# Optimization experiments

Hardware: AMD Instinct MI355X
Metric: run time of the kernel (lower is better)

Reference implementation:

```python
import jax, jax.numpy as jnp
import numpy as np

B, S, D, V, K, H, L, U = 256, 50, 32, 10000, 16, 64, 2, 32
NORM = 0.01


def setup_inputs() -> dict:
    key = jax.random.key(0)
    ks = iter(jax.random.split(key, 64))
    r = lambda *sh: jax.random.normal(next(ks), sh, dtype=jnp.float32) * 0.05
    inp = {
        'x1': r(B, U), 'z1': r(B, S, D), 'x2': r(B, U), 'z2': r(B, S, D),
        'embd': r(V, D),
        'dec_w1': r(D, H), 'dec_b1': r(H), 'dec_w2': r(H, D), 'dec_b2': r(D),
        'i_wih': r(3 * D, D), 'i_whh': r(3 * D, D), 'i_bih': r(3 * D), 'i_bhh': r(3 * D),
        'c_wih': r(3 * D, D), 'c_whh': r(3 * D, D), 'c_bih': r(3 * D), 'c_bhh': r(3 * D),
        'im_w1': r(D, D), 'im_b1': r(D), 'im_w2': r(D, D), 'im_b2': r(D),
        'cm_w1': r(D, D), 'cm_b1': r(D), 'cm_w2': r(D, D), 'cm_b2': r(D),
        'hw1': r(L, D, K * K), 'hb1': r(L, K * K), 'hw2': r(L, D, K * K), 'hb2': r(L, K * K),
        'lin_w': r(L, U, K), 'lin_b': r(L, K), 'lout_w': r(L, K, U), 'lout_b': r(L, U),
        'sample_num': B, 'trigger_seq_length': 30,
    }
    return inp


def _gru(x, wih, whh, bih, bhh):
    # PyTorch GRU, batch_first, h0 = 0; gate order (r, z, n)
    gi = jnp.einsum('bsd,ed->bse', x, wih) + bih  # [B,S,3D]

    def step(h, gi_t):
        gh = h @ whh.T + bhh
        gir, giz, gin = jnp.split(gi_t, 3, axis=-1)
        ghr, ghz, ghn = jnp.split(gh, 3, axis=-1)
        rr = jax.nn.sigmoid(gir + ghr)
        zz = jax.nn.sigmoid(giz + ghz)
        nn = jnp.tanh(gin + rr * ghn)
        h = (1.0 - zz) * nn + zz * h
        return h, h

    h0 = jnp.zeros((x.shape[0], whh.shape[1]), x.dtype)
    _, hs = jax.lax.scan(step, h0, jnp.swapaxes(gi, 0, 1))
    return jnp.swapaxes(hs, 0, 1)  # [B,S,D]


def _forward(x1, z1, x2, z2, embd, dec_w1, dec_b1, dec_w2, dec_b2,
             i_wih, i_whh, i_bih, i_bhh, c_wih, c_whh, c_bih, c_bhh,
             im_w1, im_b1, im_w2, im_b2, cm_w1, cm_b1, cm_w2, cm_b2,
             hw1, hb1, hw2, hb2, lin_w, lin_b, lout_w, lout_b,
             sample_num, trigger_seq_length):
    # --- VQVAE.find_nearest: cdist + argmin + gather (index path has no grad) ---
    q = jax.lax.stop_gradient(z1)
    t = jax.lax.stop_gradient(embd)
    # ||q - t||^2 expanded; argmin over sqrt == argmin over squared dist
    d2 = ((q * q).sum(-1)[:, :, None]
          - 2.0 * jnp.einsum('bsd,vd->bsv', q, t)
          + (t * t).sum(-1)[None, None, :])  # [B,S,V]
    idx = jnp.argmin(d2, axis=2)  # [B,S]
    z_emb = embd[idx]  # [B,S,D], gradient flows into embd via gather

    # --- VQVAE.decode ---
    h = jax.nn.leaky_relu(z_emb @ dec_w1 + dec_b1, negative_slope=0.1)
    z_recon = h @ dec_w2 + dec_b2  # [B,S,D]

    total_loss = jnp.mean((z2 - jax.lax.stop_gradient(z_emb)) ** 2)

    # --- item branch: GRU -> pick trigger step -> MLP (tanh, linear) ---
    hs = _gru(z_recon, i_wih, i_whh, i_bih, i_bhh)
    u1 = hs[:, trigger_seq_length, :]
    z1f = jnp.tanh(u1 @ im_w1 + im_b1) @ im_w2 + im_b2  # [B,D]

    # --- category branch ---
    hs = _gru(z2, c_wih, c_whh, c_bih, c_bhh)
    u2 = hs[:, trigger_seq_length, :]
    z2f = jnp.tanh(u2 @ cm_w1 + cm_b1) @ cm_w2 + cm_b2  # [B,D]

    # --- hypernetwork layers (activations in self.modules are never applied) ---
    out = x1
    for i in range(L):
        iw = (z1f @ hw1[i] + hb1[i]).reshape(sample_num, K, K)
        cw = (z2f @ hw2[i] + hb2[i]).reshape(sample_num, K, K)
        w = jnp.clip(iw, -NORM, NORM) + cw  # [B,K,K]
        out = out @ lin_w[i] + lin_b[i]  # [B,K]
        out = jnp.einsum('bk,bkj->bj', out, w)  # bmm
        out = out @ lout_w[i] + lout_b[i]  # [B,U]
    return out, total_loss


def reference(x1, z1, x2, z2, embd, dec_w1, dec_b1, dec_w2, dec_b2,
              i_wih, i_whh, i_bih, i_bhh, c_wih, c_whh, c_bih, c_bhh,
              im_w1, im_b1, im_w2, im_b2, cm_w1, cm_b1, cm_w2, cm_b2,
              hw1, hb1, hw2, hb2, lin_w, lin_b, lout_w, lout_b,
              sample_num, trigger_seq_length):
    return _forward(x1, z1, x2, z2, embd, dec_w1, dec_b1, dec_w2, dec_b2,
                    i_wih, i_whh, i_bih, i_bhh, c_wih, c_whh, c_bih, c_bhh,
                    im_w1, im_b1, im_w2, im_b2, cm_w1, cm_b1, cm_w2, cm_b2,
                    hw1, hb1, hw2, hb2, lin_w, lin_b, lout_w, lout_b,
                    sample_num, trigger_seq_length)
```

## Files before the change

### kernel.cpp

```cpp
#include <hip/hip_runtime.h>
#include <math.h>

#define B 256
#define S 50
#define D 32
#define V 10000
#define VPAD 10240
#define KK 16
#define HH 64
#define LL 2
#define UU 32
#define TT 30
#define NROWS (B*S)
#define NORMC 0.01f
#define CH 256
#define NSLICE 10
#define SLICE_V 1024
#define VQ_RB 128

typedef __attribute__((ext_vector_type(8))) short bf16x8;
typedef __attribute__((ext_vector_type(4))) float f32x4;

__device__ __forceinline__ float sigmoidf_(float x) { return 1.0f / (1.0f + expf(-x)); }

__device__ __forceinline__ unsigned short f2bf(float x) {
    union { float f; unsigned int u; } a; a.f = x;
    unsigned int u = a.u;
    return (unsigned short)((u + 0x7FFFu + ((u >> 16) & 1u)) >> 16);
}
__device__ __forceinline__ float bf2f(unsigned short h) {
    union { unsigned int u; float f; } a; a.u = ((unsigned int)h) << 16; return a.f;
}

__device__ __forceinline__ void gld16(void* lds, const void* g) {
    __builtin_amdgcn_global_load_lds(
        (const __attribute__((address_space(1))) unsigned int*)g,
        (__attribute__((address_space(3))) unsigned int*)lds, 16, 0, 0);
}
__device__ __forceinline__ void gld4(void* lds, const void* g) {
    __builtin_amdgcn_global_load_lds(
        (const __attribute__((address_space(1))) unsigned int*)g,
        (__attribute__((address_space(3))) unsigned int*)lds, 4, 0, 0);
}

__global__ __launch_bounds__(256) void k_prep(const float* __restrict__ embd,
                                              const float* __restrict__ z1,
                                              unsigned short* __restrict__ Eh, unsigned short* __restrict__ El,
                                              unsigned short* __restrict__ Qh, unsigned short* __restrict__ Ql,
                                              float* __restrict__ tn, float* __restrict__ loss_sum,
                                              unsigned int* __restrict__ cnt) {
    int gid = blockIdx.x * 256 + threadIdx.x;
    if (gid == 0) loss_sum[0] = 0.f;
    if (gid == 1) cnt[0] = 0u;
    if (gid >= VPAD * 4 + 4 * NROWS) return;
    int isRow = (gid >= VPAD * 4);
    if (!isRow) {
        int item = gid >> 2, qd = gid & 3;
        unsigned short* dh = Eh + (size_t)item * D + qd * 8;
        unsigned short* dl = El + (size_t)item * D + qd * 8;
        if (item >= V) {
            unsigned short z[8] = {0, 0, 0, 0, 0, 0, 0, 0};
            *(uint4*)dh = *(const uint4*)z;
            *(uint4*)dl = *(const uint4*)z;
            if (qd == 0) tn[item] = INFINITY;
            return;
        }
        const float* src = embd + (size_t)item * D + qd * 8;
        float4 x0 = *(const float4*)(src);
        float4 x1 = *(const float4*)(src + 4);
        float xs[8] = {x0.x, x0.y, x0.z, x0.w, x1.x, x1.y, x1.z, x1.w};
        unsigned short hv[8], lv[8];
        float ss = 0.f;
#pragma unroll
        for (int i = 0; i < 8; i++) {
            float x = xs[i];
            ss = fmaf(x, x, ss);
            unsigned short h = f2bf(x);
            hv[i] = h;
            lv[i] = f2bf(x - bf2f(h));
        }
        *(uint4*)dh = *(const uint4*)hv;
        *(uint4*)dl = *(const uint4*)lv;
        ss += __shfl_xor(ss, 1);
        ss += __shfl_xor(ss, 2);
        if (qd == 0) tn[item] = 0.5f * ss;
    } else {
        int g = gid - VPAD * 4;
        int item = g >> 2, qd = g & 3;
        const float* src = z1 + (size_t)item * D + qd * 8;
        unsigned short* dh = Qh + (size_t)item * D + qd * 8;
        unsigned short* dl = Ql + (size_t)item * D + qd * 8;
        float4 x0 = *(const float4*)(src);
        float4 x1 = *(const float4*)(src + 4);
        float xs[8] = {x0.x, x0.y, x0.z, x0.w, x1.x, x1.y, x1.z, x1.w};
        unsigned short hv[8], lv[8];
#pragma unroll
        for (int i = 0; i < 8; i++) {
            float x = -xs[i];
            unsigned short h = f2bf(x);
            hv[i] = h;
            lv[i] = f2bf(x - bf2f(h));
        }
        *(uint4*)dh = *(const uint4*)hv;
        *(uint4*)dl = *(const uint4*)lv;
    }
}

__global__ __launch_bounds__(256, 4) void k_vq(const short* __restrict__ Qh, const short* __restrict__ Ql,
                                               const short* __restrict__ Eh, const short* __restrict__ El,
                                               const float* __restrict__ tn,
                                               float2* __restrict__ pbsv) {
    __shared__ __attribute__((aligned(16))) short EhL[CH * 32];
    __shared__ __attribute__((aligned(16))) short ElL[CH * 32];
    __shared__ float tnL[CH];
    const int tid = threadIdx.x;
    const int wave = tid >> 6, lane = tid & 63;
    const int rg = blockIdx.x / NSLICE, slice = blockIdx.x % NSLICE;
    const int row0 = rg * VQ_RB;
    const int quad = lane >> 4, c15 = lane & 15;
    const int swz = quad ^ ((c15 >> 1) & 3);
    const int ar0 = row0 + wave * 32 + c15;
    bf16x8 ah0 = *(const bf16x8*)(Qh + (size_t)ar0 * 32 + quad * 8);
    bf16x8 al0 = *(const bf16x8*)(Ql + (size_t)ar0 * 32 + quad * 8);
    bf16x8 ah1 = *(const bf16x8*)(Qh + (size_t)(ar0 + 16) * 32 + quad * 8);
    bf16x8 al1 = *(const bf16x8*)(Ql + (size_t)(ar0 + 16) * 32 + quad * 8);
    float best0[4], best1[4]; int bv0[4], bv1[4];
#pragma unroll
    for (int i = 0; i < 4; i++) {
        best0[i] = INFINITY; best1[i] = INFINITY;
        bv0[i] = 0x7fffffff; bv1[i] = 0x7fffffff;
    }
    const int vbeg = slice * SLICE_V;
    for (int c0 = 0; c0 < SLICE_V; c0 += CH) {
        __syncthreads();
        {
            const int sbS = (vbeg + c0) * 32;
#pragma unroll
            for (int i = 0; i < 4; i++) {
                int c = wave * 256 + i * 64 + lane;
                int code = c >> 2;
                int q = (c & 3) ^ ((c >> 3) & 3);
                int srcOff = sbS + code * 32 + q * 8;
                int dstOff = (wave * 256 + i * 64) * 8;
                gld16(EhL + dstOff, Eh + srcOff);
                gld16(ElL + dstOff, El + srcOff);
            }
            gld4(tnL + wave * 64, tn + vbeg + c0 + wave * 64 + lane);
        }
        __syncthreads();
#pragma unroll
        for (int t = 0; t < 16; t++) {
            const int code = t * 16 + c15;
            const int boff = code * 32 + swz * 8;
            bf16x8 bh = *(const bf16x8*)(EhL + boff);
            bf16x8 bl = *(const bf16x8*)(ElL + boff);
            const float tnv = tnL[code];
            f32x4 acc0 = {tnv, tnv, tnv, tnv};
            f32x4 acc1 = {tnv, tnv, tnv, tnv};
            acc0 = __builtin_amdgcn_mfma_f32_16x16x32_bf16(ah0, bh, acc0, 0, 0, 0);
            acc1 = __builtin_amdgcn_mfma_f32_16x16x32_bf16(ah1, bh, acc1, 0, 0, 0);
            acc0 = __builtin_amdgcn_mfma_f32_16x16x32_bf16(al0, bh, acc0, 0, 0, 0);
            acc1 = __builtin_amdgcn_mfma_f32_16x16x32_bf16(al1, bh, acc1, 0, 0, 0);
            acc0 = __builtin_amdgcn_mfma_f32_16x16x32_bf16(ah0, bl, acc0, 0, 0, 0);
            acc1 = __builtin_amdgcn_mfma_f32_16x16x32_bf16(ah1, bl, acc1, 0, 0, 0);
            const int v = vbeg + c0 + code;
#pragma unroll
            for (int i = 0; i < 4; i++) {
                float s0 = acc0[i];
                if (s0 < best0[i]) { best0[i] = s0; bv0[i] = v; }
                float s1 = acc1[i];
                if (s1 < best1[i]) { best1[i] = s1; bv1[i] = v; }
            }
        }
    }
#pragma unroll
    for (int m = 1; m <= 8; m <<= 1) {
#pragma unroll
        for (int i = 0; i < 4; i++) {
            float os = __shfl_xor(best0[i], m); int ov = __shfl_xor(bv0[i], m);
            if (os < best0[i] || (os == best0[i] && ov < bv0[i])) { best0[i] = os; bv0[i] = ov; }
            os = __shfl_xor(best1[i], m); ov = __shfl_xor(bv1[i], m);
            if (os < best1[i] || (os == best1[i] && ov < bv1[i])) { best1[i] = os; bv1[i] = ov; }
        }
    }
    if (c15 == 0) {
#pragma unroll
        for (int i = 0; i < 4; i++) {
            int r0 = row0 + wave * 32 + quad * 4 + i;
            float2 p0; p0.x = best0[i]; p0.y = __int_as_float(bv0[i]);
            pbsv[(size_t)r0 * NSLICE + slice] = p0;
            int r1 = r0 + 16;
            float2 p1; p1.x = best1[i]; p1.y = __int_as_float(bv1[i]);
            pbsv[(size_t)r1 * NSLICE + slice] = p1;
        }
    }
}

__global__ __launch_bounds__(256) void k_fused(
        const float* __restrict__ x1, const float* __restrict__ z2,
        const float* __restrict__ embd, const float2* __restrict__ pbsv,
        const float* __restrict__ dw1, const float* __restrict__ db1,
        const float* __restrict__ dw2, const float* __restrict__ db2,
        const float* __restrict__ i_wih, const float* __restrict__ i_whh,
        const float* __restrict__ i_bih, const float* __restrict__ i_bhh,
        const float* __restrict__ c_wih, const float* __restrict__ c_whh,
        const float* __restrict__ c_bih, const float* __restrict__ c_bhh,
        const float* __restrict__ im_w1, const float* __restrict__ im_b1,
        const float* __restrict__ im_w2, const float* __restrict__ im_b2,
        const float* __restrict__ cm_w1, const float* __restrict__ cm_b1,
        const float* __restrict__ cm_w2, const float* __restrict__ cm_b2,
        const float* __restrict__ hw1, const float* __restrict__ hb1,
        const float* __restrict__ hw2, const float* __restrict__ hb2,
        const float* __restrict__ lin_w, const float* __restrict__ lin_b,
        const float* __restrict__ lout_w, const float* __restrict__ lout_b,
        float* __restrict__ loss_sum, unsigned int* __restrict__ cnt,
        float* __restrict__ out) {
    __shared__ float zeL[50][33];
    __shared__ float dw1L[2048], dw2L[2048];
    __shared__ float db1L[64], db2L[32];
    __shared__ __attribute__((aligned(16))) float xsi[TT + 1][32];
    __shared__ float gii[TT + 1][96], gic[TT + 1][96];
    __shared__ float aL[TT + 1][65];
    __shared__ __attribute__((aligned(16))) float hI[2][32], hC[2][32];
    __shared__ float ghI[96], ghC[96];
    __shared__ float afL[2][32];
    __shared__ float z1fL[32], z2fL[32];
    __shared__ float wW[512];
    __shared__ float t1s[16], t2s[16], ocs[32];
    __shared__ int   vidL[50];
    __shared__ float lossRed[4];
    const int tid = threadIdx.x;
    const int b = blockIdx.x;
    const float* z2b = z2 + (size_t)b * (S * D);

    for (int p = tid; p < 2048; p += 256) { dw1L[p] = dw1[p]; dw2L[p] = dw2[p]; }
    if (tid < 64) db1L[tid] = db1[tid];
    if (tid >= 64 && tid < 96) db2L[tid - 64] = db2[tid - 64];
    if (tid < 50) {
        const float2* pp = pbsv + (size_t)(b * S + tid) * NSLICE;
        float bs = INFINITY; int bv = 0x7fffffff;
#pragma unroll
        for (int j = 0; j < NSLICE; j++) {
            float2 p = pp[j];
            int v = __float_as_int(p.y);
            if (p.x < bs) { bs = p.x; bv = v; }
        }
        vidL[tid] = bv;
    }
    __syncthreads();
    {
        const int q = tid & 7;
#pragma unroll
        for (int it = 0; it < 2; it++) {
            int s = it * 32 + (tid >> 3);
            if (s < 50) {
                float4 e4 = *(const float4*)(embd + (size_t)vidL[s] * D + q * 4);
                zeL[s][q * 4 + 0] = e4.x; zeL[s][q * 4 + 1] = e4.y;
                zeL[s][q * 4 + 2] = e4.z; zeL[s][q * 4 + 3] = e4.w;
            }
        }
    }
    __syncthreads();
    {
        const int q = tid & 7;
        float ls = 0.f;
#pragma unroll
        for (int it = 0; it < 2; it++) {
            int s = it * 32 + (tid >> 3);
            if (s < 50) {
                float4 x4 = *(const float4*)(z2b + s * D + q * 4);
                float d0 = x4.x - zeL[s][q * 4 + 0], d1 = x4.y - zeL[s][q * 4 + 1];
                float d2 = x4.z - zeL[s][q * 4 + 2], d3 = x4.w - zeL[s][q * 4 + 3];
                ls += d0 * d0 + d1 * d1 + d2 * d2 + d3 * d3;
            }
        }
#pragma unroll
        for (int off = 32; off > 0; off >>= 1) ls += __shfl_down(ls, off);
        if ((tid & 63) == 0) lossRed[tid >> 6] = ls;
        const int s = tid >> 3;
        if (s <= TT) {
#pragma unroll
            for (int j = 0; j < 8; j++) {
                int h = q * 8 + j;
                float a = db1L[h];
#pragma unroll
                for (int d = 0; d < 32; d++) a = fmaf(zeL[s][d], dw1L[d * 64 + h], a);
                aL[s][h] = (a >= 0.f) ? a : 0.1f * a;
            }
        }
    }
    __syncthreads();
    if (tid == 0) atomicAdd(loss_sum, lossRed[0] + lossRed[1] + lossRed[2] + lossRed[3]);
    {
        const int s = tid >> 3, q = tid & 7;
        if (s <= TT) {
            float zr[4];
#pragma unroll
            for (int dd = 0; dd < 4; dd++) zr[dd] = db2L[q * 4 + dd];
            for (int h = 0; h < 64; h++) {
                float av = aL[s][h];
#pragma unroll
                for (int dd = 0; dd < 4; dd++) zr[dd] = fmaf(av, dw2L[h * 32 + q * 4 + dd], zr[dd]);
            }
            float4 o4 = make_float4(zr[0], zr[1], zr[2], zr[3]);
            *(float4*)&xsi[s][q * 4] = o4;
        }
    }
    __syncthreads();
    const bool actG = (tid < 96) || (tid >= 128 && tid < 224);
    const int gru = (tid >= 128) ? 1 : 0;
    const int e = gru ? (tid - 128) : tid;
    if (actG) {
        float wihRow[32];
        const float* wg = gru ? c_wih : i_wih;
#pragma unroll
        for (int d = 0; d < 32; d++) wihRow[d] = wg[e * 32 + d];
        const float bi = (gru ? c_bih : i_bih)[e];
        float* giP = gru ? &gic[0][0] : &gii[0][0];
        for (int s = 0; s <= TT; s++) {
            float g = bi;
            if (gru) {
                const float4* xp = (const float4*)(z2b + s * D);
#pragma unroll
                for (int k = 0; k < 8; k++) {
                    float4 xv = xp[k];
                    g = fmaf(xv.x, wihRow[4 * k + 0], g);
                    g = fmaf(xv.y, wihRow[4 * k + 1], g);
                    g = fmaf(xv.z, wihRow[4 * k + 2], g);
                    g = fmaf(xv.w, wihRow[4 * k + 3], g);
                }
            } else {
                const float4* xp = (const float4*)&xsi[s][0];
#pragma unroll
                for (int k = 0; k < 8; k++) {
                    float4 xv = xp[k];
                    g = fmaf(xv.x, wihRow[4 * k + 0], g);
                    g = fmaf(xv.y, wihRow[4 * k + 1], g);
                    g = fmaf(xv.z, wihRow[4 * k + 2], g);
                    g = fmaf(xv.w, wihRow[4 * k + 3], g);
                }
            }
            giP[s * 96 + e] = g;
        }
    }
    float whhRow[32]; float bh = 0.f;
    if (actG) {
        const float* wg = gru ? c_whh : i_whh;
#pragma unroll
        for (int d = 0; d < 32; d++) whhRow[d] = wg[e * 32 + d];
        bh = (gru ? c_bhh : i_bhh)[e];
    }
    if (tid < 64) { (tid < 32 ? hI[0] : hC[0])[tid & 31] = 0.f; }
    __syncthreads();
    for (int t = 0; t <= TT; t++) {
        const int cur = t & 1;
        if (actG) {
            float g = bh;
            const float4* hp = (const float4*)(gru ? &hC[cur][0] : &hI[cur][0]);
#pragma unroll
            for (int k = 0; k < 8; k++) {
                float4 hv = hp[k];
                g = fmaf(hv.x, whhRow[4 * k + 0], g);
                g = fmaf(hv.y, whhRow[4 * k + 1], g);
                g = fmaf(hv.z, whhRow[4 * k + 2], g);
                g = fmaf(hv.w, whhRow[4 * k + 3], g);
            }
            (gru ? ghC : ghI)[e] = g;
        }
        __syncthreads();
        if (tid < 64) {
            const int g2 = tid >> 5, l = tid & 31;
            const float* giP = g2 ? &gic[t][0] : &gii[t][0];
            const float* ghP = g2 ? ghC : ghI;
            float* hP = g2 ? &hC[0][0] : &hI[0][0];
            float rr = sigmoidf_(giP[l] + ghP[l]);
            float zz = sigmoidf_(giP[l + 32] + ghP[l + 32]);
            float nn = tanhf(giP[l + 64] + rr * ghP[l + 64]);
            hP[(1 - cur) * 32 + l] = (1.f - zz) * nn + zz * hP[cur * 32 + l];
        }
        __syncthreads();
    }
    {
        const bool actM = (tid < 32) || (tid >= 128 && tid < 160);
        const int g2 = (tid >= 128) ? 1 : 0;
        const int l = tid & 31;
        if (actM) {
            const float* w1 = g2 ? cm_w1 : im_w1;
            const float* b1 = g2 ? cm_b1 : im_b1;
            const float* hP = g2 ? &hC[1][0] : &hI[1][0];
            float a = b1[l];
#pragma unroll
            for (int d = 0; d < 32; d++) a = fmaf(hP[d], w1[d * 32 + l], a);
            afL[g2][l] = tanhf(a);
        }
        __syncthreads();
        if (actM) {
            const float* w2 = g2 ? cm_w2 : im_w2;
            const float* b2 = g2 ? cm_b2 : im_b2;
            float o = b2[l];
#pragma unroll
            for (int d = 0; d < 32; d++) o = fmaf(afL[g2][d], w2[d * 32 + l], o);
            (g2 ? z2fL : z1fL)[l] = o;
        }
        if (tid < 32) ocs[tid] = x1[b * 32 + tid];
    }
    __syncthreads();
    {
        const int kk = tid;
#pragma unroll
        for (int ly = 0; ly < LL; ly++) {
            float a = hb1[ly * 256 + kk], c = hb2[ly * 256 + kk];
            const float* h1 = hw1 + ly * 8192 + kk;
            const float* h2 = hw2 + ly * 8192 + kk;
#pragma unroll
            for (int d = 0; d < 32; d++) {
                a = fmaf(z1fL[d], h1[d * 256], a);
                c = fmaf(z2fL[d], h2[d * 256], c);
            }
            a = fminf(fmaxf(a, -NORMC), NORMC);
            wW[ly * 256 + kk] = a + c;
        }
    }
    __syncthreads();
#pragma unroll
    for (int i = 0; i < LL; i++) {
        if (tid < 16) {
            float a = lin_b[i * 16 + tid];
#pragma unroll
            for (int u = 0; u < 32; u++) a = fmaf(ocs[u], lin_w[i * 512 + u * 16 + tid], a);
            t1s[tid] = a;
        }
        __syncthreads();
        if (tid < 16) {
            float a = 0.f;
#pragma unroll
            for (int k = 0; k < 16; k++) a = fmaf(t1s[k], wW[i * 256 + k * 16 + tid], a);
            t2s[tid] = a;
        }
        __syncthreads();
        if (tid < 32) {
            float a = lout_b[i * 32 + tid];
#pragma unroll
            for (int k = 0; k < 16; k++) a = fmaf(t2s[k], lout_w[i * 512 + k * 32 + tid], a);
            ocs[tid] = a;
        }
        __syncthreads();
    }
    if (tid < 32) out[(size_t)b * 32 + tid] = ocs[tid];
    if (tid == 0) {
        __threadfence();
        unsigned int old = atomicAdd(cnt, 1u);
        if (old == B - 1) {
            float tot = atomicAdd(loss_sum, 0.0f);
            out[B * UU] = tot * (1.0f / (float)(B * S * D));
        }
    }
}

extern "C" void kernel_launch(void* const* d_in, const int* in_sizes, int n_in,
                              void* d_out, int out_size, void* d_ws, size_t ws_size,
                              hipStream_t stream) {
    const float* x1     = (const float*)d_in[0];
    const float* z1     = (const float*)d_in[1];
    const float* z2     = (const float*)d_in[3];
    const float* embd   = (const float*)d_in[4];
    const float* dec_w1 = (const float*)d_in[5];
    const float* dec_b1 = (const float*)d_in[6];
    const float* dec_w2 = (const float*)d_in[7];
    const float* dec_b2 = (const float*)d_in[8];
    const float* i_wih  = (const float*)d_in[9];
    const float* i_whh  = (const float*)d_in[10];
    const float* i_bih  = (const float*)d_in[11];
    const float* i_bhh  = (const float*)d_in[12];
    const float* c_wih  = (const float*)d_in[13];
    const float* c_whh  = (const float*)d_in[14];
    const float* c_bih  = (const float*)d_in[15];
    const float* c_bhh  = (const float*)d_in[16];
    const float* im_w1  = (const float*)d_in[17];
    const float* im_b1  = (const float*)d_in[18];
    const float* im_w2  = (const float*)d_in[19];
    const float* im_b2  = (const float*)d_in[20];
    const float* cm_w1  = (const float*)d_in[21];
    const float* cm_b1  = (const float*)d_in[22];
    const float* cm_w2  = (const float*)d_in[23];
    const float* cm_b2  = (const float*)d_in[24];
    const float* hw1    = (const float*)d_in[25];
    const float* hb1    = (const float*)d_in[26];
    const float* hw2    = (const float*)d_in[27];
    const float* hb2    = (const float*)d_in[28];
    const float* lin_w  = (const float*)d_in[29];
    const float* lin_b  = (const float*)d_in[30];
    const float* lout_w = (const float*)d_in[31];
    const float* lout_b = (const float*)d_in[32];

    float* wsf      = (float*)d_ws;
    float* loss_sum = wsf;
    unsigned int* cnt = (unsigned int*)(wsf + 1);
    float* tn       = wsf + 64;
    float2* pbsv    = (float2*)(wsf + 10304);
    unsigned short* Eh = (unsigned short*)(wsf + 266304);
    unsigned short* El = (unsigned short*)(wsf + 430144);
    unsigned short* Qh = (unsigned short*)(wsf + 593984);
    unsigned short* Ql = (unsigned short*)(wsf + 798784);

    k_prep<<<(VPAD * 4 + 4 * NROWS + 255) / 256, 256, 0, stream>>>(embd, z1, Eh, El, Qh, Ql,
                                                                   tn, loss_sum, cnt);
    k_vq<<<(NROWS / VQ_RB) * NSLICE, 256, 0, stream>>>((const short*)Qh, (const short*)Ql,
                                                       (const short*)Eh, (const short*)El, tn, pbsv);
    k_fused<<<B, 256, 0, stream>>>(x1, z2, embd, pbsv,
                                   dec_w1, dec_b1, dec_w2, dec_b2,
                                   i_wih, i_whh, i_bih, i_bhh,
                                   c_wih, c_whh, c_bih, c_bhh,
                                   im_w1, im_b1, im_w2, im_b2,
                                   cm_w1, cm_b1, cm_w2, cm_b2,
                                   hw1, hb1, hw2, hb2,
                                   lin_w, lin_b, lout_w, lout_b,
                                   loss_sum, cnt, (float*)d_out);
}
```

Baseline: 196.7 us.

## Fuse query bf16 split into VQ kernel and load whole code slice once

The hi/lo bf16 split of the query rows moves from the prep kernel into the VQ search kernel, so the Qh/Ql workspace buffers and their global round-trip go away. The VQ kernel now uses 20 slices of 512 codes, each loaded into LDS in one shot with a single barrier instead of a chunked loop. Code norms are read straight into registers, and the block order is now slice-major. The cost is twice the LDS per block and more registers, which can lower occupancy, and each query row is now split redundantly by every slice block.

```diff
diff --git a/kernel.cpp b/kernel.cpp
--- a/kernel.cpp
+++ b/kernel.cpp
@@ -13,10 +13,11 @@
 #define TT 30
 #define NROWS (B*S)
 #define NORMC 0.01f
-#define CH 256
-#define NSLICE 10
-#define SLICE_V 1024
+#define NSLICE 20
+#define SLICE_V 512
+#define NTILES 32
 #define VQ_RB 128
+#define NRG (NROWS / VQ_RB)
 
 typedef __attribute__((ext_vector_type(8))) short bf16x8;
 typedef __attribute__((ext_vector_type(4))) float f32x4;
@@ -37,140 +38,122 @@
         (const __attribute__((address_space(1))) unsigned int*)g,
         (__attribute__((address_space(3))) unsigned int*)lds, 16, 0, 0);
 }
-__device__ __forceinline__ void gld4(void* lds, const void* g) {
-    __builtin_amdgcn_global_load_lds(
-        (const __attribute__((address_space(1))) unsigned int*)g,
-        (__attribute__((address_space(3))) unsigned int*)lds, 4, 0, 0);
-}
 
 __global__ __launch_bounds__(256) void k_prep(const float* __restrict__ embd,
-                                              const float* __restrict__ z1,
                                               unsigned short* __restrict__ Eh, unsigned short* __restrict__ El,
-                                              unsigned short* __restrict__ Qh, unsigned short* __restrict__ Ql,
                                               float* __restrict__ tn, float* __restrict__ loss_sum,
                                               unsigned int* __restrict__ cnt) {
     int gid = blockIdx.x * 256 + threadIdx.x;
     if (gid == 0) loss_sum[0] = 0.f;
     if (gid == 1) cnt[0] = 0u;
-    if (gid >= VPAD * 4 + 4 * NROWS) return;
-    int isRow = (gid >= VPAD * 4);
-    if (!isRow) {
-        int item = gid >> 2, qd = gid & 3;
-        unsigned short* dh = Eh + (size_t)item * D + qd * 8;
-        unsigned short* dl = El + (size_t)item * D + qd * 8;
-        if (item >= V) {
-            unsigned short z[8] = {0, 0, 0, 0, 0, 0, 0, 0};
-            *(uint4*)dh = *(const uint4*)z;
-            *(uint4*)dl = *(const uint4*)z;
-            if (qd == 0) tn[item] = INFINITY;
-            return;
-        }
-        const float* src = embd + (size_t)item * D + qd * 8;
-        float4 x0 = *(const float4*)(src);
-        float4 x1 = *(const float4*)(src + 4);
-        float xs[8] = {x0.x, x0.y, x0.z, x0.w, x1.x, x1.y, x1.z, x1.w};
-        unsigned short hv[8], lv[8];
-        float ss = 0.f;
+    if (gid >= VPAD * 4) return;
+    int item = gid >> 2, qd = gid & 3;
+    unsigned short* dh = Eh + (size_t)item * D + qd * 8;
+    unsigned short* dl = El + (size_t)item * D + qd * 8;
+    if (item >= V) {
+        unsigned short z[8] = {0, 0, 0, 0, 0, 0, 0, 0};
+        *(uint4*)dh = *(const uint4*)z;
+        *(uint4*)dl = *(const uint4*)z;
+        if (qd == 0) tn[item] = INFINITY;
+        return;
+    }
+    const float* src = embd + (size_t)item * D + qd * 8;
+    float4 x0 = *(const float4*)(src);
+    float4 x1 = *(const float4*)(src + 4);
+    float xs[8] = {x0.x, x0.y, x0.z, x0.w, x1.x, x1.y, x1.z, x1.w};
+    unsigned short hv[8], lv[8];
+    float ss = 0.f;
+#pragma unroll
+    for (int i = 0; i < 8; i++) {
+        float x = xs[i];
+        ss = fmaf(x, x, ss);
+        unsigned short h = f2bf(x);
+        hv[i] = h;
+        lv[i] = f2bf(x - bf2f(h));
+    }
+    *(uint4*)dh = *(const uint4*)hv;
+    *(uint4*)dl = *(const uint4*)lv;
+    ss += __shfl_xor(ss, 1);
+    ss += __shfl_xor(ss, 2);
+    if (qd == 0) tn[item] = 0.5f * ss;
+}
+
+__global__ __launch_bounds__(256) void k_vq(const float* __restrict__ z1,
+                                            const short* __restrict__ Eh, const short* __restrict__ El,
+                                            const float* __restrict__ tn,
+                                            float2* __restrict__ pbsv) {
+    __shared__ __attribute__((aligned(16))) short EhL[SLICE_V * 32];
+    __shared__ __attribute__((aligned(16))) short ElL[SLICE_V * 32];
+    const int tid = threadIdx.x;
+    const int wave = tid >> 6, lane = tid & 63;
+    const int slice = blockIdx.x / NRG, rg = blockIdx.x % NRG;
+    const int row0 = rg * VQ_RB;
+    const int quad = lane >> 4, c15 = lane & 15;
+    const int swz = quad ^ ((c15 >> 1) & 3);
+    const int vbeg = slice * SLICE_V;
+    {
 #pragma unroll
         for (int i = 0; i < 8; i++) {
-            float x = xs[i];
-            ss = fmaf(x, x, ss);
-            unsigned short h = f2bf(x);
-            hv[i] = h;
-            lv[i] = f2bf(x - bf2f(h));
-        }
-        *(uint4*)dh = *(const uint4*)hv;
-        *(uint4*)dl = *(const uint4*)lv;
-        ss += __shfl_xor(ss, 1);
-        ss += __shfl_xor(ss, 2);
-        if (qd == 0) tn[item] = 0.5f * ss;
-    } else {
-        int g = gid - VPAD * 4;
-        int item = g >> 2, qd = g & 3;
-        const float* src = z1 + (size_t)item * D + qd * 8;
-        unsigned short* dh = Qh + (size_t)item * D + qd * 8;
-        unsigned short* dl = Ql + (size_t)item * D + qd * 8;
-        float4 x0 = *(const float4*)(src);
-        float4 x1 = *(const float4*)(src + 4);
-        float xs[8] = {x0.x, x0.y, x0.z, x0.w, x1.x, x1.y, x1.z, x1.w};
-        unsigned short hv[8], lv[8];
+            int c = wave * 512 + i * 64 + lane;
+            int code = c >> 2;
+            int q = (c & 3) ^ ((c >> 3) & 3);
+            int srcOff = (vbeg + code) * 32 + q * 8;
+            int dstOff = (wave * 512 + i * 64) * 8;
+            gld16(EhL + dstOff, Eh + srcOff);
+            gld16(ElL + dstOff, El + srcOff);
+        }
+    }
+    const int ar0 = row0 + wave * 32 + c15;
+    bf16x8 ah0, al0, ah1, al1;
+#pragma unroll
+    for (int rt = 0; rt < 2; rt++) {
+        const float* qp = z1 + (size_t)(ar0 + rt * 16) * 32 + quad * 8;
+        float4 x0 = *(const float4*)qp;
+        float4 x1v = *(const float4*)(qp + 4);
+        float xs[8] = {x0.x, x0.y, x0.z, x0.w, x1v.x, x1v.y, x1v.z, x1v.w};
+        short hv[8], lv[8];
 #pragma unroll
         for (int i = 0; i < 8; i++) {
             float x = -xs[i];
             unsigned short h = f2bf(x);
-            hv[i] = h;
-            lv[i] = f2bf(x - bf2f(h));
-        }
-        *(uint4*)dh = *(const uint4*)hv;
-        *(uint4*)dl = *(const uint4*)lv;
-    }
-}
-
-__global__ __launch_bounds__(256, 4) void k_vq(const short* __restrict__ Qh, const short* __restrict__ Ql,
-                                               const short* __restrict__ Eh, const short* __restrict__ El,
-                                               const float* __restrict__ tn,
-                                               float2* __restrict__ pbsv) {
-    __shared__ __attribute__((aligned(16))) short EhL[CH * 32];
-    __shared__ __attribute__((aligned(16))) short ElL[CH * 32];
-    __shared__ float tnL[CH];
-    const int tid = threadIdx.x;
-    const int wave = tid >> 6, lane = tid & 63;
-    const int rg = blockIdx.x / NSLICE, slice = blockIdx.x % NSLICE;
-    const int row0 = rg * VQ_RB;
-    const int quad = lane >> 4, c15 = lane & 15;
-    const int swz = quad ^ ((c15 >> 1) & 3);
-    const int ar0 = row0 + wave * 32 + c15;
-    bf16x8 ah0 = *(const bf16x8*)(Qh + (size_t)ar0 * 32 + quad * 8);
-    bf16x8 al0 = *(const bf16x8*)(Ql + (size_t)ar0 * 32 + quad * 8);
-    bf16x8 ah1 = *(const bf16x8*)(Qh + (size_t)(ar0 + 16) * 32 + quad * 8);
-    bf16x8 al1 = *(const bf16x8*)(Ql + (size_t)(ar0 + 16) * 32 + quad * 8);
+            hv[i] = (short)h;
+            lv[i] = (short)f2bf(x - bf2f(h));
+        }
+        if (rt == 0) { ah0 = *(const bf16x8*)hv; al0 = *(const bf16x8*)lv; }
+        else         { ah1 = *(const bf16x8*)hv; al1 = *(const bf16x8*)lv; }
+    }
+    float tnr[NTILES];
+#pragma unroll
+    for (int t = 0; t < NTILES; t++) tnr[t] = tn[vbeg + t * 16 + c15];
     float best0[4], best1[4]; int bv0[4], bv1[4];
 #pragma unroll
     for (int i = 0; i < 4; i++) {
         best0[i] = INFINITY; best1[i] = INFINITY;
         bv0[i] = 0x7fffffff; bv1[i] = 0x7fffffff;
     }
-    const int vbeg = slice * SLICE_V;
-    for (int c0 = 0; c0 < SLICE_V; c0 += CH) {
-        __syncthreads();
-        {
-            const int sbS = (vbeg + c0) * 32;
-#pragma unroll
-            for (int i = 0; i < 4; i++) {
-                int c = wave * 256 + i * 64 + lane;
-                int code = c >> 2;
-                int q = (c & 3) ^ ((c >> 3) & 3);
-                int srcOff = sbS + code * 32 + q * 8;
-                int dstOff = (wave * 256 + i * 64) * 8;
-                gld16(EhL + dstOff, Eh + srcOff);
-                gld16(ElL + dstOff, El + srcOff);
-            }
-            gld4(tnL + wave * 64, tn + vbeg + c0 + wave * 64 + lane);
-        }
-        __syncthreads();
-#pragma unroll
-        for (int t = 0; t < 16; t++) {
-            const int code = t * 16 + c15;
-            const int boff = code * 32 + swz * 8;
-            bf16x8 bh = *(const bf16x8*)(EhL + boff);
-            bf16x8 bl = *(const bf16x8*)(ElL + boff);
-            const float tnv = tnL[code];
-            f32x4 acc0 = {tnv, tnv, tnv, tnv};
-            f32x4 acc1 = {tnv, tnv, tnv, tnv};
-            acc0 = __builtin_amdgcn_mfma_f32_16x16x32_bf16(ah0, bh, acc0, 0, 0, 0);
-            acc1 = __builtin_amdgcn_mfma_f32_16x16x32_bf16(ah1, bh, acc1, 0, 0, 0);
-            acc0 = __builtin_amdgcn_mfma_f32_16x16x32_bf16(al0, bh, acc0, 0, 0, 0);
-            acc1 = __builtin_amdgcn_mfma_f32_16x16x32_bf16(al1, bh, acc1, 0, 0, 0);
-            acc0 = __builtin_amdgcn_mfma_f32_16x16x32_bf16(ah0, bl, acc0, 0, 0, 0);
-            acc1 = __builtin_amdgcn_mfma_f32_16x16x32_bf16(ah1, bl, acc1, 0, 0, 0);
-            const int v = vbeg + c0 + code;
-#pragma unroll
-            for (int i = 0; i < 4; i++) {
-                float s0 = acc0[i];
-                if (s0 < best0[i]) { best0[i] = s0; bv0[i] = v; }
-                float s1 = acc1[i];
-                if (s1 < best1[i]) { best1[i] = s1; bv1[i] = v; }
-            }
+    __syncthreads();
+#pragma unroll
+    for (int t = 0; t < NTILES; t++) {
+        const int code = t * 16 + c15;
+        const int boff = code * 32 + swz * 8;
+        bf16x8 bh = *(const bf16x8*)(EhL + boff);
+        bf16x8 bl = *(const bf16x8*)(ElL + boff);
+        const float tnv = tnr[t];
+        f32x4 acc0 = {tnv, tnv, tnv, tnv};
+        f32x4 acc1 = {tnv, tnv, tnv, tnv};
+        acc0 = __builtin_amdgcn_mfma_f32_16x16x32_bf16(ah0, bh, acc0, 0, 0, 0);
+        acc1 = __builtin_amdgcn_mfma_f32_16x16x32_bf16(ah1, bh, acc1, 0, 0, 0);
+        acc0 = __builtin_amdgcn_mfma_f32_16x16x32_bf16(al0, bh, acc0, 0, 0, 0);
+        acc1 = __builtin_amdgcn_mfma_f32_16x16x32_bf16(al1, bh, acc1, 0, 0, 0);
+        acc0 = __builtin_amdgcn_mfma_f32_16x16x32_bf16(ah0, bl, acc0, 0, 0, 0);
+        acc1 = __builtin_amdgcn_mfma_f32_16x16x32_bf16(ah1, bl, acc1, 0, 0, 0);
+        const int v = vbeg + code;
+#pragma unroll
+        for (int i = 0; i < 4; i++) {
+            float s0 = acc0[i];
+            if (s0 < best0[i]) { best0[i] = s0; bv0[i] = v; }
+            float s1 = acc1[i];
+            if (s1 < best1[i]) { best1[i] = s1; bv1[i] = v; }
         }
     }
 #pragma unroll
@@ -498,15 +481,11 @@
     unsigned int* cnt = (unsigned int*)(wsf + 1);
     float* tn       = wsf + 64;
     float2* pbsv    = (float2*)(wsf + 10304);
-    unsigned short* Eh = (unsigned short*)(wsf + 266304);
-    unsigned short* El = (unsigned short*)(wsf + 430144);
-    unsigned short* Qh = (unsigned short*)(wsf + 593984);
-    unsigned short* Ql = (unsigned short*)(wsf + 798784);
-
-    k_prep<<<(VPAD * 4 + 4 * NROWS + 255) / 256, 256, 0, stream>>>(embd, z1, Eh, El, Qh, Ql,
-                                                                   tn, loss_sum, cnt);
-    k_vq<<<(NROWS / VQ_RB) * NSLICE, 256, 0, stream>>>((const short*)Qh, (const short*)Ql,
-                                                       (const short*)Eh, (const short*)El, tn, pbsv);
+    unsigned short* Eh = (unsigned short*)(wsf + 522304);
+    unsigned short* El = (unsigned short*)(wsf + 686144);
+
+    k_prep<<<(VPAD * 4 + 255) / 256, 256, 0, stream>>>(embd, Eh, El, tn, loss_sum, cnt);
+    k_vq<<<NSLICE * NRG, 256, 0, stream>>>(z1, (const short*)Eh, (const short*)El, tn, pbsv);
     k_fused<<<B, 256, 0, stream>>>(x1, z2, embd, pbsv,
                                    dec_w1, dec_b1, dec_w2, dec_b2,
                                    i_wih, i_whh, i_bih, i_bhh,
```

Result: slower. 238.2 us (+21.1%).
